# Kernel tuning notes

Hardware: AMD Instinct MI355X
Metric: run time of the kernel (lower is better)

Reference implementation:

```python
import jax, jax.numpy as jnp
import numpy as np

B, OBS, D_MODEL, D_STATE, D_CONV, EXPAND, ACT = 2048, 512, 1024, 16, 4, 2, 18
D_INNER = EXPAND * D_MODEL            # 2048
DT_RANK = (D_MODEL + 15) // 16        # 64

def setup_inputs() -> dict:
    key = jax.random.key(0)
    ks = jax.random.split(key, 20)
    s = 0.02
    return {
        "obs": jax.random.normal(ks[0], (B, OBS), jnp.float32),
        "conv_state": jax.random.normal(ks[1], (B, D_INNER, D_CONV), jnp.float32),
        "ssm_state": jax.random.normal(ks[2], (B, D_INNER, D_STATE), jnp.float32),
        # obs -> d_model projection
        "in_proj_w": jax.random.normal(ks[3], (D_MODEL, OBS), jnp.float32) * s,
        "in_proj_b": jnp.zeros((D_MODEL,), jnp.float32),
        # Mamba in_proj (no bias): d_model -> 2*d_inner (x and z)
        "mamba_in_w": jax.random.normal(ks[4], (2 * D_INNER, D_MODEL), jnp.float32) * s,
        # depthwise causal conv
        "conv_w": jax.random.normal(ks[5], (D_INNER, D_CONV), jnp.float32) * s,
        "conv_b": jnp.zeros((D_INNER,), jnp.float32),
        # x_proj (no bias): d_inner -> dt_rank + 2*d_state
        "x_proj_w": jax.random.normal(ks[6], (DT_RANK + 2 * D_STATE, D_INNER), jnp.float32) * s,
        # dt_proj: dt_rank -> d_inner
        "dt_w": jax.random.normal(ks[7], (D_INNER, DT_RANK), jnp.float32) * s,
        "dt_b": jax.random.normal(ks[8], (D_INNER,), jnp.float32) * s,
        # S4D-style A init: A_log = log(A), A in [1, d_state]
        "A_log": jnp.log(jnp.broadcast_to(jnp.arange(1, D_STATE + 1, dtype=jnp.float32), (D_INNER, D_STATE)) + 0.0),
        "D": jnp.ones((D_INNER,), jnp.float32),
        # out_proj (no bias): d_inner -> d_model
        "out_proj_w": jax.random.normal(ks[9], (D_MODEL, D_INNER), jnp.float32) * s,
        # actor / critic heads
        "pol_w": jax.random.normal(ks[10], (ACT, D_MODEL), jnp.float32) * s,
        "pol_b": jnp.zeros((ACT,), jnp.float32),
        "val_w": jax.random.normal(ks[11], (1, D_MODEL), jnp.float32) * s,
        "val_b": jnp.zeros((1,), jnp.float32),
    }

def _silu(x):
    return x * jax.nn.sigmoid(x)

def reference(obs, conv_state, ssm_state, in_proj_w, in_proj_b, mamba_in_w,
              conv_w, conv_b, x_proj_w, dt_w, dt_b, A_log, D, out_proj_w,
              pol_w, pol_b, val_w, val_b):
    # obs projection: [B, d_model]
    h = obs @ in_proj_w.T + in_proj_b
    # Mamba step (single timestep)
    xz = h @ mamba_in_w.T                        # [B, 2*d_inner]
    x, z = xz[:, :D_INNER], xz[:, D_INNER:]
    # causal depthwise conv via shifted conv_state buffer
    conv_state_new = jnp.concatenate([conv_state[:, :, 1:], x[:, :, None]], axis=-1)  # [B, d_inner, d_conv]
    x = _silu(jnp.sum(conv_state_new * conv_w[None], axis=-1) + conv_b)               # [B, d_inner]
    # input-dependent dt, B, C
    x_db = x @ x_proj_w.T                        # [B, dt_rank + 2*d_state]
    dt = x_db[:, :DT_RANK]
    Bmat = x_db[:, DT_RANK:DT_RANK + D_STATE]    # [B, d_state]
    Cmat = x_db[:, DT_RANK + D_STATE:]           # [B, d_state]
    dt = jax.nn.softplus(dt @ dt_w.T + dt_b)     # [B, d_inner]
    A = -jnp.exp(A_log)                          # [d_inner, d_state]
    dA = jnp.exp(dt[:, :, None] * A[None])       # [B, d_inner, d_state]
    dB = dt[:, :, None] * Bmat[:, None, :]       # [B, d_inner, d_state]
    ssm_state_new = ssm_state * dA + x[:, :, None] * dB
    y = jnp.einsum('bdn,bn->bd', ssm_state_new, Cmat) + D * x
    y = y * _silu(z)
    out = y @ out_proj_w.T                       # [B, d_model]
    logits = out @ pol_w.T + pol_b               # [B, action_dim]
    value = out @ val_w.T + val_b                # [B, 1]
    return logits, value, conv_state_new, ssm_state_new
```

## Files before the change

kernel.cpp:

```cpp
#include <hip/hip_runtime.h>
#include <hip/hip_bf16.h>
#include <math.h>


#define BATCH 2048
#define OBSD 512
#define DMODEL 1024
#define DINNER 2048
#define DSTATE 16
#define DTRANK 64
#define NACT 18

typedef __attribute__((ext_vector_type(8))) short shortx8;
typedef __attribute__((ext_vector_type(4))) float floatx4;

__device__ inline float sig_(float x) { return 1.f / (1.f + __expf(-x)); }

__device__ inline unsigned short bfc(float x) {
    __hip_bfloat16 h = __float2bfloat16(x);
    return *(unsigned short*)&h;
}

__device__ inline void store_bf4(unsigned short* dst, float4 v) {
    ushort4 u;
    u.x = bfc(v.x); u.y = bfc(v.y); u.z = bfc(v.z); u.w = bfc(v.w);
    *(ushort4*)dst = u;
}

__global__ __launch_bounds__(256) void convert_kernel(
    const float* __restrict__ obs, const float* __restrict__ w1,
    const float* __restrict__ w2, const float* __restrict__ w3,
    const float* __restrict__ w5, const float* __restrict__ Alog,
    unsigned short* __restrict__ obs_bf, unsigned short* __restrict__ w1_bf,
    unsigned short* __restrict__ w2_bf, unsigned short* __restrict__ w3_bf,
    unsigned short* __restrict__ w5_bf, float* __restrict__ A_neg)
{
    int g = blockIdx.x * 256 + threadIdx.x;
    if (g < 262144) {
        store_bf4(obs_bf + g * 4, ((const float4*)obs)[g]);
    } else if (g < 393216) {
        int t = g - 262144;
        store_bf4(w1_bf + t * 4, ((const float4*)w1)[t]);
    } else if (g < 1441792) {
        int t = g - 393216;
        store_bf4(w2_bf + t * 4, ((const float4*)w2)[t]);
    } else if (g < 1507328) {
        int t = g - 1441792;
        int e = t * 4;
        int n = e >> 11;
        int k = e & 2047;
        float4 v = {0.f, 0.f, 0.f, 0.f};
        if (n < 96) v = *(const float4*)(w3 + n * 2048 + k);
        store_bf4(w3_bf + e, v);
    } else if (g < 2031616) {
        int t = g - 1507328;
        store_bf4(w5_bf + t * 4, ((const float4*)w5)[t]);
    } else {
        int t = g - 2031616;
        float4 v = ((const float4*)Alog)[t];
        float4 o = {-__expf(v.x), -__expf(v.y), -__expf(v.z), -__expf(v.w)};
        ((float4*)A_neg)[t] = o;
    }
}

template <int BF16OUT, int BIAS, int SPLITK>
__global__ __launch_bounds__(256) void gemm_bt(
    const short* __restrict__ A, const short* __restrict__ Bm,
    void* __restrict__ Cout, const float* __restrict__ bias,
    int M, int N, int K, int ksplit_len)
{
    __shared__ short As[128 * 32];
    __shared__ short Bs[128 * 32];

    const int tid  = threadIdx.x;
    const int wave = tid >> 6;
    const int lane = tid & 63;
    const int quad = lane >> 4;
    const int l16  = lane & 15;
    const int wm   = (wave & 1) << 6;
    const int wn   = (wave >> 1) << 6;
    const int bm   = blockIdx.x;
    const int bn   = blockIdx.y;

    int kbeg = 0, kend = K;
    if (SPLITK) { kbeg = blockIdx.z * ksplit_len; kend = kbeg + ksplit_len; }

    floatx4 acc[4][4] = {};

    const int v0 = tid * 8;
    const int r0 = v0 >> 5, c0 = v0 & 31;
    const int v1 = (256 + tid) * 8;
    const int r1 = v1 >> 5, c1 = v1 & 31;

    const short* Abase = A + (size_t)bm * 128 * K;
    const short* Bbase = Bm + (size_t)bn * 128 * K;

    for (int k0 = kbeg; k0 < kend; k0 += 32) {
        __syncthreads();
        __builtin_amdgcn_global_load_lds(
            (const __attribute__((address_space(1))) unsigned int*)(Abase + (size_t)r0 * K + k0 + c0),
            (__attribute__((address_space(3))) unsigned int*)(As + wave * 512), 16, 0, 0);
        __builtin_amdgcn_global_load_lds(
            (const __attribute__((address_space(1))) unsigned int*)(Abase + (size_t)r1 * K + k0 + c1),
            (__attribute__((address_space(3))) unsigned int*)(As + 2048 + wave * 512), 16, 0, 0);
        __builtin_amdgcn_global_load_lds(
            (const __attribute__((address_space(1))) unsigned int*)(Bbase + (size_t)r0 * K + k0 + c0),
            (__attribute__((address_space(3))) unsigned int*)(Bs + wave * 512), 16, 0, 0);
        __builtin_amdgcn_global_load_lds(
            (const __attribute__((address_space(1))) unsigned int*)(Bbase + (size_t)r1 * K + k0 + c1),
            (__attribute__((address_space(3))) unsigned int*)(Bs + 2048 + wave * 512), 16, 0, 0);
        __syncthreads();

        shortx8 af[4], bfv[4];
#pragma unroll
        for (int i = 0; i < 4; ++i)
            af[i] = *(const shortx8*)(As + (wm + i * 16 + l16) * 32 + quad * 8);
#pragma unroll
        for (int j = 0; j < 4; ++j)
            bfv[j] = *(const shortx8*)(Bs + (wn + j * 16 + l16) * 32 + quad * 8);
#pragma unroll
        for (int i = 0; i < 4; ++i)
#pragma unroll
            for (int j = 0; j < 4; ++j)
                acc[i][j] = __builtin_amdgcn_mfma_f32_16x16x32_bf16(af[i], bfv[j], acc[i][j], 0, 0, 0);
    }

    if (BF16OUT) {
        unsigned short* C = (unsigned short*)Cout;
#pragma unroll
        for (int i = 0; i < 4; ++i) {
            int gm = bm * 128 + wm + i * 16 + quad * 4;
#pragma unroll
            for (int j = 0; j < 4; ++j) {
                int gn = bn * 128 + wn + j * 16 + l16;
                float bv = BIAS ? bias[gn] : 0.f;
#pragma unroll
                for (int r = 0; r < 4; ++r)
                    C[(size_t)(gm + r) * N + gn] = bfc(acc[i][j][r] + bv);
            }
        }
    } else {
        float* C = (float*)Cout;
        if (SPLITK) C += (size_t)blockIdx.z * M * N;
#pragma unroll
        for (int i = 0; i < 4; ++i) {
            int gm = bm * 128 + wm + i * 16 + quad * 4;
#pragma unroll
            for (int j = 0; j < 4; ++j) {
                int gn = bn * 128 + wn + j * 16 + l16;
                float bv = BIAS ? bias[gn] : 0.f;
#pragma unroll
                for (int r = 0; r < 4; ++r)
                    C[(size_t)(gm + r) * N + gn] = acc[i][j][r] + bv;
            }
        }
    }
}

__global__ __launch_bounds__(256) void conv_kernel(
    const float* __restrict__ xz, const float* __restrict__ conv_state,
    const float* __restrict__ conv_w, const float* __restrict__ conv_b,
    float* __restrict__ conv_out, float* __restrict__ x_conv,
    unsigned short* __restrict__ x_conv_bf)
{
    int idx = blockIdx.x * 256 + threadIdx.x;
    int b = idx >> 11, d = idx & 2047;
    float4 cs = *(const float4*)(conv_state + (size_t)idx * 4);
    float x = xz[(size_t)b * 4096 + d];
    float4 w = *(const float4*)(conv_w + d * 4);
    float s = cs.y * w.x + cs.z * w.y + cs.w * w.z + x * w.w + conv_b[d];
    float xc = s * sig_(s);
    float4 outv = {cs.y, cs.z, cs.w, x};
    *(float4*)(conv_out + (size_t)idx * 4) = outv;
    x_conv[idx] = xc;
    x_conv_bf[idx] = bfc(xc);
}

__global__ __launch_bounds__(256) void reduce_g3(
    const float* __restrict__ part, float* __restrict__ x_db)
{
    int idx = blockIdx.x * 256 + threadIdx.x;
    int b = idx / 96, n = idx - b * 96;
    float s = 0.f;
#pragma unroll
    for (int z = 0; z < 8; ++z)
        s += part[(size_t)z * BATCH * 128 + b * 128 + n];
    x_db[idx] = s;
}

__global__ __launch_bounds__(256) void dt_kernel(
    const float* __restrict__ x_db, const float* __restrict__ dt_w,
    const float* __restrict__ dt_b, float* __restrict__ dt_full)
{
    __shared__ float dtp[64];
    int b = blockIdx.y;
    int d = blockIdx.x * 256 + threadIdx.x;
    if (threadIdx.x < 64) dtp[threadIdx.x] = x_db[b * 96 + threadIdx.x];
    __syncthreads();
    float acc = dt_b[d];
    const float4* w = (const float4*)(dt_w + d * 64);
#pragma unroll
    for (int k4 = 0; k4 < 16; ++k4) {
        float4 wv = w[k4];
        acc += dtp[k4 * 4 + 0] * wv.x + dtp[k4 * 4 + 1] * wv.y +
               dtp[k4 * 4 + 2] * wv.z + dtp[k4 * 4 + 3] * wv.w;
    }
    float sp = acc > 20.f ? acc : log1pf(__expf(acc));
    dt_full[(size_t)b * 2048 + d] = sp;
}

__global__ __launch_bounds__(256) void ssm_kernel(
    const float* __restrict__ ssm_state, const float* __restrict__ x_conv,
    const float* __restrict__ dt_full, const float* __restrict__ xz,
    const float* __restrict__ x_db, const float* __restrict__ A_neg,
    const float* __restrict__ Dvec, float* __restrict__ ssm_out,
    unsigned short* __restrict__ y_bf)
{
    __shared__ float BC[32];
    int b = blockIdx.y;
    int d = blockIdx.x * 256 + threadIdx.x;
    if (threadIdx.x < 32) BC[threadIdx.x] = x_db[b * 96 + 64 + threadIdx.x];
    __syncthreads();
    int idx = b * 2048 + d;
    float x  = x_conv[idx];
    float dt = dt_full[idx];
    float z  = xz[(size_t)b * 4096 + 2048 + d];
    float xdt = x * dt;
    float y = 0.f;
    const float4* Sv = (const float4*)(ssm_state + (size_t)idx * 16);
    const float4* Av = (const float4*)(A_neg + d * 16);
    float4* So = (float4*)(ssm_out + (size_t)idx * 16);
#pragma unroll
    for (int q = 0; q < 4; ++q) {
        float4 s = Sv[q];
        float4 a = Av[q];
        float4 o;
        o.x = s.x * __expf(dt * a.x) + xdt * BC[q * 4 + 0];
        o.y = s.y * __expf(dt * a.y) + xdt * BC[q * 4 + 1];
        o.z = s.z * __expf(dt * a.z) + xdt * BC[q * 4 + 2];
        o.w = s.w * __expf(dt * a.w) + xdt * BC[q * 4 + 3];
        So[q] = o;
        y += o.x * BC[16 + q * 4 + 0] + o.y * BC[16 + q * 4 + 1] +
             o.z * BC[16 + q * 4 + 2] + o.w * BC[16 + q * 4 + 3];
    }
    y += Dvec[d] * x;
    y *= z * sig_(z);
    y_bf[idx] = bfc(y);
}

__global__ __launch_bounds__(256) void heads_kernel(
    const float* __restrict__ out, const float* __restrict__ pol_w,
    const float* __restrict__ pol_b, const float* __restrict__ val_w,
    const float* __restrict__ val_b, float* __restrict__ logits,
    float* __restrict__ value)
{
    __shared__ float row[1024];
    int b = blockIdx.x;
    int tid = threadIdx.x;
    ((float4*)row)[tid] = ((const float4*)(out + (size_t)b * 1024))[tid];
    __syncthreads();
    int wave = tid >> 6, lane = tid & 63;
    for (int j = wave; j < 19; j += 4) {
        const float* w = (j < 18) ? (pol_w + j * 1024) : val_w;
        float p = 0.f;
        for (int k = lane; k < 1024; k += 64) p += row[k] * w[k];
#pragma unroll
        for (int off = 32; off; off >>= 1) p += __shfl_down(p, off);
        if (lane == 0) {
            if (j < 18) logits[b * NACT + j] = p + pol_b[j];
            else        value[b] = p + val_b[0];
        }
    }
}

extern "C" void kernel_launch(void* const* d_in, const int* in_sizes, int n_in,
                              void* d_out, int out_size, void* d_ws, size_t ws_size,
                              hipStream_t stream)
{
    const float* obs        = (const float*)d_in[0];
    const float* conv_state = (const float*)d_in[1];
    const float* ssm_state  = (const float*)d_in[2];
    const float* in_proj_w  = (const float*)d_in[3];
    const float* in_proj_b  = (const float*)d_in[4];
    const float* mamba_in_w = (const float*)d_in[5];
    const float* conv_w     = (const float*)d_in[6];
    const float* conv_b     = (const float*)d_in[7];
    const float* x_proj_w   = (const float*)d_in[8];
    const float* dt_w       = (const float*)d_in[9];
    const float* dt_b       = (const float*)d_in[10];
    const float* A_log      = (const float*)d_in[11];
    const float* Dvec       = (const float*)d_in[12];
    const float* out_proj_w = (const float*)d_in[13];
    const float* pol_w      = (const float*)d_in[14];
    const float* pol_b      = (const float*)d_in[15];
    const float* val_w      = (const float*)d_in[16];
    const float* val_b      = (const float*)d_in[17];

    char* ws = (char*)d_ws;
    unsigned short* obs_bf    = (unsigned short*)(ws + 0);
    unsigned short* w1_bf     = (unsigned short*)(ws + 2097152);
    unsigned short* w2_bf     = (unsigned short*)(ws + 3145728);
    unsigned short* w3_bf     = (unsigned short*)(ws + 11534336);
    unsigned short* w5_bf     = (unsigned short*)(ws + 12058624);
    float*          A_neg     = (float*)(ws + 16252928);
    unsigned short* h_bf      = (unsigned short*)(ws + 16384000);
    float*          xz        = (float*)(ws + 20578304);
    float*          x_conv    = (float*)(ws + 54132736);
    unsigned short* x_conv_bf = (unsigned short*)(ws + 70909952);
    float*          g3_part   = (float*)(ws + 79298560);
    float*          x_db      = (float*)(ws + 87687168);
    float*          dt_full   = (float*)(ws + 88473600);
    unsigned short* y_bf      = (unsigned short*)(ws + 105250816);
    float*          outb      = (float*)(ws + 113639424);
    if (ws_size < 122028032) return;

    float* logits   = (float*)d_out;
    float* value    = logits + (size_t)BATCH * NACT;
    float* conv_out = value + BATCH;
    float* ssm_out  = conv_out + (size_t)BATCH * DINNER * 4;

    convert_kernel<<<7968, 256, 0, stream>>>(obs, in_proj_w, mamba_in_w, x_proj_w,
                                             out_proj_w, A_log, obs_bf, w1_bf, w2_bf,
                                             w3_bf, w5_bf, A_neg);

    gemm_bt<1, 1, 0><<<dim3(16, 8), 256, 0, stream>>>(
        (const short*)obs_bf, (const short*)w1_bf, h_bf, in_proj_b, 2048, 1024, 512, 0);

    gemm_bt<0, 0, 0><<<dim3(16, 32), 256, 0, stream>>>(
        (const short*)h_bf, (const short*)w2_bf, xz, nullptr, 2048, 4096, 1024, 0);

    conv_kernel<<<16384, 256, 0, stream>>>(xz, conv_state, conv_w, conv_b,
                                           conv_out, x_conv, x_conv_bf);

    gemm_bt<0, 0, 1><<<dim3(16, 1, 8), 256, 0, stream>>>(
        (const short*)x_conv_bf, (const short*)w3_bf, g3_part, nullptr, 2048, 128, 2048, 256);
    reduce_g3<<<768, 256, 0, stream>>>(g3_part, x_db);

    dt_kernel<<<dim3(8, 2048), 256, 0, stream>>>(x_db, dt_w, dt_b, dt_full);

    ssm_kernel<<<dim3(8, 2048), 256, 0, stream>>>(ssm_state, x_conv, dt_full, xz,
                                                  x_db, A_neg, Dvec, ssm_out, y_bf);

    gemm_bt<0, 0, 0><<<dim3(16, 8), 256, 0, stream>>>(
        (const short*)y_bf, (const short*)w5_bf, outb, nullptr, 2048, 1024, 2048, 0);

    heads_kernel<<<2048, 256, 0, stream>>>(outb, pol_w, pol_b, val_w, val_b,
                                           logits, value);
}
```

Baseline: 911.9 us.

## Fuse conv into in_proj GEMM epilogue and fold out_proj into heads

The conv1d and SiLU(z) computation moves into the epilogue of the mamba in_proj GEMM, so the fp32 xz tensor no longer goes through global memory. The out_proj weight is folded algebraically into the policy/value head weights, so the 2048x1024x2048 out_proj GEMM and its weight conversion are dropped. The dt kernel now processes 8 batch rows per block to reuse weights, and the SSM kernel spreads each channel's state across 4 threads with shuffle reductions. Folding out_proj into the heads changes rounding, because the heads now read bf16 y directly against the fp32 folded weights.

```diff
diff --git a/kernel.cpp b/kernel.cpp
--- a/kernel.cpp
+++ b/kernel.cpp
@@ -30,10 +30,10 @@
 __global__ __launch_bounds__(256) void convert_kernel(
     const float* __restrict__ obs, const float* __restrict__ w1,
     const float* __restrict__ w2, const float* __restrict__ w3,
-    const float* __restrict__ w5, const float* __restrict__ Alog,
+    const float* __restrict__ Alog,
     unsigned short* __restrict__ obs_bf, unsigned short* __restrict__ w1_bf,
     unsigned short* __restrict__ w2_bf, unsigned short* __restrict__ w3_bf,
-    unsigned short* __restrict__ w5_bf, float* __restrict__ A_neg)
+    float* __restrict__ A_neg)
 {
     int g = blockIdx.x * 256 + threadIdx.x;
     if (g < 262144) {
@@ -52,11 +52,8 @@
         float4 v = {0.f, 0.f, 0.f, 0.f};
         if (n < 96) v = *(const float4*)(w3 + n * 2048 + k);
         store_bf4(w3_bf + e, v);
-    } else if (g < 2031616) {
+    } else {
         int t = g - 1507328;
-        store_bf4(w5_bf + t * 4, ((const float4*)w5)[t]);
-    } else {
-        int t = g - 2031616;
         float4 v = ((const float4*)Alog)[t];
         float4 o = {-__expf(v.x), -__expf(v.y), -__expf(v.z), -__expf(v.w)};
         ((float4*)A_neg)[t] = o;
@@ -157,23 +154,104 @@
     }
 }
 
-__global__ __launch_bounds__(256) void conv_kernel(
-    const float* __restrict__ xz, const float* __restrict__ conv_state,
-    const float* __restrict__ conv_w, const float* __restrict__ conv_b,
-    float* __restrict__ conv_out, float* __restrict__ x_conv,
-    unsigned short* __restrict__ x_conv_bf)
-{
-    int idx = blockIdx.x * 256 + threadIdx.x;
-    int b = idx >> 11, d = idx & 2047;
-    float4 cs = *(const float4*)(conv_state + (size_t)idx * 4);
-    float x = xz[(size_t)b * 4096 + d];
-    float4 w = *(const float4*)(conv_w + d * 4);
-    float s = cs.y * w.x + cs.z * w.y + cs.w * w.z + x * w.w + conv_b[d];
-    float xc = s * sig_(s);
-    float4 outv = {cs.y, cs.z, cs.w, x};
-    *(float4*)(conv_out + (size_t)idx * 4) = outv;
-    x_conv[idx] = xc;
-    x_conv_bf[idx] = bfc(xc);
+__global__ __launch_bounds__(256) void gemm_g2(
+    const short* __restrict__ A, const short* __restrict__ Bm,
+    const float* __restrict__ conv_state, const float* __restrict__ conv_w,
+    const float* __restrict__ conv_b, float* __restrict__ conv_out,
+    float* __restrict__ x_conv, unsigned short* __restrict__ x_conv_bf,
+    float* __restrict__ zs, int K)
+{
+    __shared__ short As[128 * 32];
+    __shared__ short Bs[128 * 32];
+
+    const int tid  = threadIdx.x;
+    const int wave = tid >> 6;
+    const int lane = tid & 63;
+    const int quad = lane >> 4;
+    const int l16  = lane & 15;
+    const int wm   = (wave & 1) << 6;
+    const int wn   = (wave >> 1) << 6;
+    const int bm   = blockIdx.x;
+    const int bn   = blockIdx.y;
+
+    floatx4 acc[4][4] = {};
+
+    const int v0 = tid * 8;
+    const int r0 = v0 >> 5, c0 = v0 & 31;
+    const int v1 = (256 + tid) * 8;
+    const int r1 = v1 >> 5, c1 = v1 & 31;
+
+    const short* Abase = A + (size_t)bm * 128 * K;
+    const short* Bbase = Bm + (size_t)bn * 128 * K;
+
+    for (int k0 = 0; k0 < K; k0 += 32) {
+        __syncthreads();
+        __builtin_amdgcn_global_load_lds(
+            (const __attribute__((address_space(1))) unsigned int*)(Abase + (size_t)r0 * K + k0 + c0),
+            (__attribute__((address_space(3))) unsigned int*)(As + wave * 512), 16, 0, 0);
+        __builtin_amdgcn_global_load_lds(
+            (const __attribute__((address_space(1))) unsigned int*)(Abase + (size_t)r1 * K + k0 + c1),
+            (__attribute__((address_space(3))) unsigned int*)(As + 2048 + wave * 512), 16, 0, 0);
+        __builtin_amdgcn_global_load_lds(
+            (const __attribute__((address_space(1))) unsigned int*)(Bbase + (size_t)r0 * K + k0 + c0),
+            (__attribute__((address_space(3))) unsigned int*)(Bs + wave * 512), 16, 0, 0);
+        __builtin_amdgcn_global_load_lds(
+            (const __attribute__((address_space(1))) unsigned int*)(Bbase + (size_t)r1 * K + k0 + c1),
+            (__attribute__((address_space(3))) unsigned int*)(Bs + 2048 + wave * 512), 16, 0, 0);
+        __syncthreads();
+
+        shortx8 af[4], bfv[4];
+#pragma unroll
+        for (int i = 0; i < 4; ++i)
+            af[i] = *(const shortx8*)(As + (wm + i * 16 + l16) * 32 + quad * 8);
+#pragma unroll
+        for (int j = 0; j < 4; ++j)
+            bfv[j] = *(const shortx8*)(Bs + (wn + j * 16 + l16) * 32 + quad * 8);
+#pragma unroll
+        for (int i = 0; i < 4; ++i)
+#pragma unroll
+            for (int j = 0; j < 4; ++j)
+                acc[i][j] = __builtin_amdgcn_mfma_f32_16x16x32_bf16(af[i], bfv[j], acc[i][j], 0, 0, 0);
+    }
+
+    if (bn < 16) {
+#pragma unroll
+        for (int j = 0; j < 4; ++j) {
+            int d = bn * 128 + wn + j * 16 + l16;
+            float4 w4 = *(const float4*)(conv_w + d * 4);
+            float cb = conv_b[d];
+#pragma unroll
+            for (int i = 0; i < 4; ++i) {
+                int gm = bm * 128 + wm + i * 16 + quad * 4;
+#pragma unroll
+                for (int r = 0; r < 4; ++r) {
+                    size_t idx = (size_t)(gm + r) * 2048 + d;
+                    float xv = acc[i][j][r];
+                    float4 cs = *(const float4*)(conv_state + idx * 4);
+                    float s = cs.y * w4.x + cs.z * w4.y + cs.w * w4.z + xv * w4.w + cb;
+                    float xc = s * sig_(s);
+                    float4 outv = {cs.y, cs.z, cs.w, xv};
+                    *(float4*)(conv_out + idx * 4) = outv;
+                    x_conv[idx] = xc;
+                    x_conv_bf[idx] = bfc(xc);
+                }
+            }
+        }
+    } else {
+#pragma unroll
+        for (int j = 0; j < 4; ++j) {
+            int d = bn * 128 + wn + j * 16 + l16 - 2048;
+#pragma unroll
+            for (int i = 0; i < 4; ++i) {
+                int gm = bm * 128 + wm + i * 16 + quad * 4;
+#pragma unroll
+                for (int r = 0; r < 4; ++r) {
+                    float zv = acc[i][j][r];
+                    zs[(size_t)(gm + r) * 2048 + d] = zv * sig_(zv);
+                }
+            }
+        }
+    }
 }
 
 __global__ __launch_bounds__(256) void reduce_g3(
@@ -192,78 +270,116 @@
     const float* __restrict__ x_db, const float* __restrict__ dt_w,
     const float* __restrict__ dt_b, float* __restrict__ dt_full)
 {
-    __shared__ float dtp[64];
-    int b = blockIdx.y;
-    int d = blockIdx.x * 256 + threadIdx.x;
-    if (threadIdx.x < 64) dtp[threadIdx.x] = x_db[b * 96 + threadIdx.x];
+    __shared__ float dtp[8][64];
+    int tid = threadIdx.x;
+    int b0 = blockIdx.y * 8;
+    {
+        int bb = tid >> 5, k = tid & 31;
+        dtp[bb][k]      = x_db[(b0 + bb) * 96 + k];
+        dtp[bb][k + 32] = x_db[(b0 + bb) * 96 + k + 32];
+    }
     __syncthreads();
-    float acc = dt_b[d];
+    int d = blockIdx.x * 256 + tid;
+    float acc[8];
+    float bv = dt_b[d];
+#pragma unroll
+    for (int bb = 0; bb < 8; ++bb) acc[bb] = bv;
     const float4* w = (const float4*)(dt_w + d * 64);
 #pragma unroll
     for (int k4 = 0; k4 < 16; ++k4) {
         float4 wv = w[k4];
-        acc += dtp[k4 * 4 + 0] * wv.x + dtp[k4 * 4 + 1] * wv.y +
-               dtp[k4 * 4 + 2] * wv.z + dtp[k4 * 4 + 3] * wv.w;
-    }
-    float sp = acc > 20.f ? acc : log1pf(__expf(acc));
-    dt_full[(size_t)b * 2048 + d] = sp;
+#pragma unroll
+        for (int bb = 0; bb < 8; ++bb) {
+            acc[bb] += dtp[bb][k4 * 4 + 0] * wv.x + dtp[bb][k4 * 4 + 1] * wv.y +
+                       dtp[bb][k4 * 4 + 2] * wv.z + dtp[bb][k4 * 4 + 3] * wv.w;
+        }
+    }
+#pragma unroll
+    for (int bb = 0; bb < 8; ++bb) {
+        float a = acc[bb];
+        float sp = a > 20.f ? a : log1pf(__expf(a));
+        dt_full[(size_t)(b0 + bb) * 2048 + d] = sp;
+    }
 }
 
 __global__ __launch_bounds__(256) void ssm_kernel(
     const float* __restrict__ ssm_state, const float* __restrict__ x_conv,
-    const float* __restrict__ dt_full, const float* __restrict__ xz,
+    const float* __restrict__ dt_full, const float* __restrict__ zs,
     const float* __restrict__ x_db, const float* __restrict__ A_neg,
     const float* __restrict__ Dvec, float* __restrict__ ssm_out,
     unsigned short* __restrict__ y_bf)
 {
     __shared__ float BC[32];
     int b = blockIdx.y;
-    int d = blockIdx.x * 256 + threadIdx.x;
-    if (threadIdx.x < 32) BC[threadIdx.x] = x_db[b * 96 + 64 + threadIdx.x];
+    int tid = threadIdx.x;
+    if (tid < 32) BC[tid] = x_db[b * 96 + 64 + tid];
     __syncthreads();
-    int idx = b * 2048 + d;
+    int q  = tid & 3;
+    int d  = blockIdx.x * 64 + (tid >> 2);
+    size_t idx = (size_t)b * 2048 + d;
     float x  = x_conv[idx];
     float dt = dt_full[idx];
-    float z  = xz[(size_t)b * 4096 + 2048 + d];
     float xdt = x * dt;
-    float y = 0.f;
-    const float4* Sv = (const float4*)(ssm_state + (size_t)idx * 16);
-    const float4* Av = (const float4*)(A_neg + d * 16);
-    float4* So = (float4*)(ssm_out + (size_t)idx * 16);
-#pragma unroll
-    for (int q = 0; q < 4; ++q) {
-        float4 s = Sv[q];
-        float4 a = Av[q];
-        float4 o;
-        o.x = s.x * __expf(dt * a.x) + xdt * BC[q * 4 + 0];
-        o.y = s.y * __expf(dt * a.y) + xdt * BC[q * 4 + 1];
-        o.z = s.z * __expf(dt * a.z) + xdt * BC[q * 4 + 2];
-        o.w = s.w * __expf(dt * a.w) + xdt * BC[q * 4 + 3];
-        So[q] = o;
-        y += o.x * BC[16 + q * 4 + 0] + o.y * BC[16 + q * 4 + 1] +
-             o.z * BC[16 + q * 4 + 2] + o.w * BC[16 + q * 4 + 3];
-    }
-    y += Dvec[d] * x;
-    y *= z * sig_(z);
-    y_bf[idx] = bfc(y);
+    float4 s = *(const float4*)(ssm_state + idx * 16 + q * 4);
+    float4 a = *(const float4*)(A_neg + d * 16 + q * 4);
+    float4 o;
+    o.x = s.x * __expf(dt * a.x) + xdt * BC[q * 4 + 0];
+    o.y = s.y * __expf(dt * a.y) + xdt * BC[q * 4 + 1];
+    o.z = s.z * __expf(dt * a.z) + xdt * BC[q * 4 + 2];
+    o.w = s.w * __expf(dt * a.w) + xdt * BC[q * 4 + 3];
+    *(float4*)(ssm_out + idx * 16 + q * 4) = o;
+    float p = o.x * BC[16 + q * 4 + 0] + o.y * BC[16 + q * 4 + 1] +
+              o.z * BC[16 + q * 4 + 2] + o.w * BC[16 + q * 4 + 3];
+    p += __shfl_xor(p, 1);
+    p += __shfl_xor(p, 2);
+    if (q == 0) {
+        float y = p + Dvec[d] * x;
+        y *= zs[idx];
+        y_bf[idx] = bfc(y);
+    }
+}
+
+__global__ __launch_bounds__(256) void fold_heads(
+    const float* __restrict__ opw, const float* __restrict__ pol_w,
+    const float* __restrict__ val_w, float* __restrict__ Wc)
+{
+    __shared__ float hw[1024];
+    int j = blockIdx.y;
+    const float* src = (j < 18) ? (pol_w + j * 1024) : val_w;
+    for (int t = threadIdx.x; t < 1024; t += 256) hw[t] = src[t];
+    __syncthreads();
+    int d = blockIdx.x * 256 + threadIdx.x;
+    float acc = 0.f;
+#pragma unroll 8
+    for (int m = 0; m < 1024; ++m)
+        acc += hw[m] * opw[(size_t)m * 2048 + d];
+    Wc[j * 2048 + d] = acc;
 }
 
 __global__ __launch_bounds__(256) void heads_kernel(
-    const float* __restrict__ out, const float* __restrict__ pol_w,
-    const float* __restrict__ pol_b, const float* __restrict__ val_w,
-    const float* __restrict__ val_b, float* __restrict__ logits,
-    float* __restrict__ value)
-{
-    __shared__ float row[1024];
+    const unsigned short* __restrict__ y_bf, const float* __restrict__ Wc,
+    const float* __restrict__ pol_b, const float* __restrict__ val_b,
+    float* __restrict__ logits, float* __restrict__ value)
+{
+    __shared__ __align__(16) float row[2048];
     int b = blockIdx.x;
     int tid = threadIdx.x;
-    ((float4*)row)[tid] = ((const float4*)(out + (size_t)b * 1024))[tid];
+    shortx8 v = ((const shortx8*)(y_bf + (size_t)b * 2048))[tid];
+#pragma unroll
+    for (int e = 0; e < 8; ++e) {
+        unsigned int u = ((unsigned int)(unsigned short)v[e]) << 16;
+        row[tid * 8 + e] = *(float*)&u;
+    }
     __syncthreads();
     int wave = tid >> 6, lane = tid & 63;
     for (int j = wave; j < 19; j += 4) {
-        const float* w = (j < 18) ? (pol_w + j * 1024) : val_w;
+        const float4* w = (const float4*)(Wc + j * 2048);
         float p = 0.f;
-        for (int k = lane; k < 1024; k += 64) p += row[k] * w[k];
+        for (int k4 = lane; k4 < 512; k4 += 64) {
+            float4 wv = w[k4];
+            float4 rv = ((const float4*)row)[k4];
+            p += rv.x * wv.x + rv.y * wv.y + rv.z * wv.z + rv.w * wv.w;
+        }
 #pragma unroll
         for (int off = 32; off; off >>= 1) p += __shfl_down(p, off);
         if (lane == 0) {
@@ -301,49 +417,44 @@
     unsigned short* w1_bf     = (unsigned short*)(ws + 2097152);
     unsigned short* w2_bf     = (unsigned short*)(ws + 3145728);
     unsigned short* w3_bf     = (unsigned short*)(ws + 11534336);
-    unsigned short* w5_bf     = (unsigned short*)(ws + 12058624);
-    float*          A_neg     = (float*)(ws + 16252928);
-    unsigned short* h_bf      = (unsigned short*)(ws + 16384000);
-    float*          xz        = (float*)(ws + 20578304);
-    float*          x_conv    = (float*)(ws + 54132736);
-    unsigned short* x_conv_bf = (unsigned short*)(ws + 70909952);
-    float*          g3_part   = (float*)(ws + 79298560);
-    float*          x_db      = (float*)(ws + 87687168);
-    float*          dt_full   = (float*)(ws + 88473600);
-    unsigned short* y_bf      = (unsigned short*)(ws + 105250816);
-    float*          outb      = (float*)(ws + 113639424);
-    if (ws_size < 122028032) return;
+    float*          A_neg     = (float*)(ws + 12058624);
+    unsigned short* h_bf      = (unsigned short*)(ws + 12189696);
+    float*          x_conv    = (float*)(ws + 16384000);
+    unsigned short* x_conv_bf = (unsigned short*)(ws + 33161216);
+    float*          zs        = (float*)(ws + 41549824);
+    float*          g3_part   = (float*)(ws + 58327040);
+    float*          x_db      = (float*)(ws + 66715648);
+    float*          dt_full   = (float*)(ws + 67502080);
+    unsigned short* y_bf      = (unsigned short*)(ws + 84279296);
+    float*          Wc        = (float*)(ws + 92667904);
+    if (ws_size < 92823552) return;
 
     float* logits   = (float*)d_out;
     float* value    = logits + (size_t)BATCH * NACT;
     float* conv_out = value + BATCH;
     float* ssm_out  = conv_out + (size_t)BATCH * DINNER * 4;
 
-    convert_kernel<<<7968, 256, 0, stream>>>(obs, in_proj_w, mamba_in_w, x_proj_w,
-                                             out_proj_w, A_log, obs_bf, w1_bf, w2_bf,
-                                             w3_bf, w5_bf, A_neg);
+    convert_kernel<<<5920, 256, 0, stream>>>(obs, in_proj_w, mamba_in_w, x_proj_w,
+                                             A_log, obs_bf, w1_bf, w2_bf, w3_bf,
+                                             A_neg);
+
+    fold_heads<<<dim3(8, 19), 256, 0, stream>>>(out_proj_w, pol_w, val_w, Wc);
 
     gemm_bt<1, 1, 0><<<dim3(16, 8), 256, 0, stream>>>(
         (const short*)obs_bf, (const short*)w1_bf, h_bf, in_proj_b, 2048, 1024, 512, 0);
 
-    gemm_bt<0, 0, 0><<<dim3(16, 32), 256, 0, stream>>>(
-        (const short*)h_bf, (const short*)w2_bf, xz, nullptr, 2048, 4096, 1024, 0);
-
-    conv_kernel<<<16384, 256, 0, stream>>>(xz, conv_state, conv_w, conv_b,
-                                           conv_out, x_conv, x_conv_bf);
+    gemm_g2<<<dim3(16, 32), 256, 0, stream>>>(
+        (const short*)h_bf, (const short*)w2_bf, conv_state, conv_w, conv_b,
+        conv_out, x_conv, x_conv_bf, zs, 1024);
 
     gemm_bt<0, 0, 1><<<dim3(16, 1, 8), 256, 0, stream>>>(
         (const short*)x_conv_bf, (const short*)w3_bf, g3_part, nullptr, 2048, 128, 2048, 256);
     reduce_g3<<<768, 256, 0, stream>>>(g3_part, x_db);
 
-    dt_kernel<<<dim3(8, 2048), 256, 0, stream>>>(x_db, dt_w, dt_b, dt_full);
-
-    ssm_kernel<<<dim3(8, 2048), 256, 0, stream>>>(ssm_state, x_conv, dt_full, xz,
-                                                  x_db, A_neg, Dvec, ssm_out, y_bf);
-
-    gemm_bt<0, 0, 0><<<dim3(16, 8), 256, 0, stream>>>(
-        (const short*)y_bf, (const short*)w5_bf, outb, nullptr, 2048, 1024, 2048, 0);
-
-    heads_kernel<<<2048, 256, 0, stream>>>(outb, pol_w, pol_b, val_w, val_b,
-                                           logits, value);
-}
+    dt_kernel<<<dim3(8, 256), 256, 0, stream>>>(x_db, dt_w, dt_b, dt_full);
+
+    ssm_kernel<<<dim3(32, 2048), 256, 0, stream>>>(ssm_state, x_conv, dt_full, zs,
+                                                   x_db, A_neg, Dvec, ssm_out, y_bf);
+
+    heads_kernel<<<2048, 256, 0, stream>>>(y_bf, Wc, pol_b, val_b, logits, value);
+}
```

New measurement: 855.6 us. -6.2%, faster.
